# Optimization experiments

Hardware: AMD Instinct MI355X
Metric: run time of the kernel (lower is better)

## Reference

```python
import jax, jax.numpy as jnp
import numpy as np

BATCH = 256
SEQ_LEN = 512
INPUT_DIM = 1
NUM_HIDDEN = 2048
NUM_CLASSES = 10


def _xavier(key, shape):
    fan_out, fan_in = shape
    limit = np.sqrt(6.0 / (fan_in + fan_out)).astype(np.float32)
    return jax.random.uniform(key, shape, jnp.float32, -limit, limit)


def setup_inputs() -> dict:
    key = jax.random.key(0)
    kx, k1, k2, k3 = jax.random.split(key, 4)
    x = jax.random.normal(kx, (BATCH, SEQ_LEN), jnp.float32)
    wph = _xavier(k1, (NUM_CLASSES, NUM_HIDDEN))
    whh = _xavier(k2, (NUM_HIDDEN, NUM_HIDDEN))
    whx = _xavier(k3, (NUM_HIDDEN, INPUT_DIM))
    bh = jnp.zeros((NUM_HIDDEN,), jnp.float32)
    bp = jnp.zeros((NUM_CLASSES,), jnp.float32)
    return {"x": x, "whx": whx, "whh": whh, "bh": bh, "wph": wph, "bp": bp}


def reference(x, whx, whh, bh, wph, bp):
    # x: [B, T] of scalar inputs (input_dim == 1)
    B = x.shape[0]
    H = whh.shape[0]
    whx_vec = whx[:, 0]  # [H]

    def step(h, xt):
        # xt: [B];  xt[:, None] @ whx.T  ==  outer(xt, whx_vec)
        h_new = jnp.tanh(xt[:, None] * whx_vec[None, :] + h @ whh.T + bh)
        return h_new, None

    h0 = jnp.zeros((B, H), x.dtype)
    h_last, _ = jax.lax.scan(step, h0, x.T)  # scan over time: [T, B]
    p = h_last @ wph.T + bp  # [B, num_classes]
    return p
```

## Files before the change

kernel.cpp:

```cpp
#include <hip/hip_runtime.h>

#define SEQL   512
#define HID    2048
#define NCLS   10

typedef _Float16 f16x8 __attribute__((ext_vector_type(8)));
typedef float    f32x4 __attribute__((ext_vector_type(4)));
typedef unsigned uintx4 __attribute__((ext_vector_type(4)));

__device__ __forceinline__ float fast_tanh(float v) {
    float e = __expf(2.0f * v);
    return 1.0f - 2.0f / (e + 1.0f);
}

__global__ void pack_w_kernel(const float* __restrict__ w, _Float16* __restrict__ o) {
    const int fid = blockIdx.x * 256 + threadIdx.x;
    int col, k0;
    if (fid < 262144) {
        const int m = fid >> 13, s5 = fid & 8191;
        const int tile = s5 >> 12, kst = (s5 >> 6) & 63, ln = s5 & 63;
        col = m * 64 + tile * 16 + (ln & 15);
        k0  = kst * 32 + (ln >> 4) * 8;
    } else {
        const int q = fid - 262144;
        const int m = q >> 13, r = q & 8191;
        const int j = r >> 10, f = (r >> 6) & 15, ln = r & 63;
        col = m * 64 + 32 + (j & 1) * 16 + (ln & 15);
        k0  = ((j >> 1) * 16 + f) * 32 + (ln >> 4) * 8;
    }
    const float* src = w + (size_t)col * HID + k0;
    f16x8 v;
    #pragma unroll
    for (int i = 0; i < 8; ++i) v[i] = (_Float16)src[i];
    *(f16x8*)(o + (size_t)fid * 8) = v;
}

__global__ void __launch_bounds__(512, 2)
rnn_main(const float* __restrict__ x, const float* __restrict__ whx,
         const _Float16* __restrict__ Wp, const float* __restrict__ bh,
         const float* __restrict__ wph, const float* __restrict__ bp,
         _Float16* __restrict__ h0, _Float16* __restrict__ h1,
         unsigned* __restrict__ ctr, float* __restrict__ out)
{
    __shared__ uint4 ldsW[8192];
    __shared__ f32x4 ldsR[16 * 64];

    const int tid = threadIdx.x;

    int xcc;
    asm volatile("s_getreg_b32 %0, hwreg(HW_REG_XCC_ID)" : "=s"(xcc));
    const int g = xcc & 7;
    unsigned* alloc   = ctr + g * 64;
    unsigned* flgbase = ctr + 512 + g * 1024;
    if (tid == 0) {
        unsigned s = __hip_atomic_fetch_add(alloc, 1u, __ATOMIC_RELAXED, __HIP_MEMORY_SCOPE_WORKGROUP);
        ((unsigned*)ldsR)[0] = s;
    }
    __syncthreads();
    const int m = (int)((unsigned*)ldsR)[0];
    unsigned* myflg = flgbase + m * 32;
    const int rowbase = g * 32;
    const int colbase = m * 64;

    const int lane = tid & 63;
    const int j    = tid >> 6;
    const int cbb  = j & 1;
    const int kq   = j >> 1;

    const uint4* P4 = (const uint4*)Wp;

    for (int s5 = tid; s5 < 8192; s5 += 512)
        ldsW[s5] = P4[m * 8192 + s5];

    for (int i = tid; i < 32 * 64; i += 512) {
        const int r = i >> 6, c = i & 63;
        const int b = rowbase + r, jj = colbase + c;
        h0[(size_t)b * HID + jj] = (_Float16)fast_tanh(x[(size_t)b * SEQL] * whx[jj] + bh[jj]);
    }

    const uint4* R4 = P4 + 262144 + m * 8192 + j * 1024 + lane;
    f16x8 bR[16];
    #pragma unroll
    for (int f = 0; f < 16; ++f) bR[f] = *(const f16x8*)&R4[f * 64];

    const int ecls = (j >> 1) & 1, ewm = j >> 2;
    const int ecol = colbase + ecls * 32 + cbb * 16 + (lane & 15);
    const float wxc = whx[ecol], bbc = bh[ecol];
    const int erow = rowbase + ewm * 16 + (lane >> 4) * 4;
    const int rdbase = ecls * 8 + cbb * 4;

    const size_t aoff = (size_t)(rowbase + (lane & 15)) * HID + (lane >> 4) * 8 + kq * 16 * 32;
    const uint4* bl = &ldsW[cbb * 4096 + kq * 16 * 64 + lane];
    const unsigned* pollp = flgbase + (lane & 31) * 32;

    __syncthreads();
    if (tid == 0)
        __hip_atomic_fetch_add(myflg, 1u, __ATOMIC_RELAXED, __HIP_MEMORY_SCOPE_WORKGROUP);

    for (int t = 1; t < SEQL; ++t) {
        const _Float16* hs = (t & 1) ? h0 : h1;
        _Float16*       hd = (t & 1) ? h1 : h0;
        const _Float16* ap  = hs + aoff;
        const _Float16* ap1 = ap + 16 * HID;

        #pragma unroll
        for (int f = 0; f < 16; ++f) asm volatile("" : "+v"(bR[f]));

        float xv[4];
        #pragma unroll
        for (int r = 0; r < 4; ++r)
            xv[r] = x[(size_t)(erow + r) * SEQL + t];

        {
            unsigned v;
            do {
                v = __hip_atomic_load(pollp, __ATOMIC_RELAXED, __HIP_MEMORY_SCOPE_AGENT);
            } while (!__all((int)(v >= (unsigned)t)));
        }
        asm volatile("buffer_inv sc0" ::: "memory");

        uintx4 av0[16], av1[16];
        #pragma unroll
        for (int f = 0; f < 16; ++f) {
            asm volatile("global_load_dwordx4 %0, %1, off"
                         : "=v"(av0[f]) : "v"(ap + f * 32));
            asm volatile("global_load_dwordx4 %0, %1, off"
                         : "=v"(av1[f]) : "v"(ap1 + f * 32));
        }
        asm volatile("s_waitcnt vmcnt(0)" ::: "memory");
        __builtin_amdgcn_sched_barrier(0);

        f32x4 aL0 = {0.f,0.f,0.f,0.f}, aL1 = aL0, aR0 = aL0, aR1 = aL0;

        #pragma unroll
        for (int f = 0; f < 16; ++f) {
            const f16x8 a0 = __builtin_bit_cast(f16x8, av0[f]);
            const f16x8 a1 = __builtin_bit_cast(f16x8, av1[f]);
            const f16x8 bLf = *(const f16x8*)&bl[f * 64];
            aL0 = __builtin_amdgcn_mfma_f32_16x16x32_f16(a0, bLf,   aL0, 0, 0, 0);
            aL1 = __builtin_amdgcn_mfma_f32_16x16x32_f16(a1, bLf,   aL1, 0, 0, 0);
            aR0 = __builtin_amdgcn_mfma_f32_16x16x32_f16(a0, bR[f], aR0, 0, 0, 0);
            aR1 = __builtin_amdgcn_mfma_f32_16x16x32_f16(a1, bR[f], aR1, 0, 0, 0);
        }

        ldsR[(cbb * 4 + kq) * 64 + lane]       = aL0;
        ldsR[(8 + cbb * 4 + kq) * 64 + lane]   = aR0;
        __syncthreads();
        if (j < 4) {
            const f32x4 s = ldsR[(rdbase + 0) * 64 + lane] + ldsR[(rdbase + 1) * 64 + lane]
                          + ldsR[(rdbase + 2) * 64 + lane] + ldsR[(rdbase + 3) * 64 + lane];
            #pragma unroll
            for (int r = 0; r < 4; ++r) {
                const int br = erow + r;
                hd[(size_t)br * HID + ecol] =
                    (_Float16)fast_tanh(s[r] + xv[r] * wxc + bbc);
            }
        }
        __syncthreads();
        ldsR[(cbb * 4 + kq) * 64 + lane]       = aL1;
        ldsR[(8 + cbb * 4 + kq) * 64 + lane]   = aR1;
        __syncthreads();
        if (j >= 4) {
            const f32x4 s = ldsR[(rdbase + 0) * 64 + lane] + ldsR[(rdbase + 1) * 64 + lane]
                          + ldsR[(rdbase + 2) * 64 + lane] + ldsR[(rdbase + 3) * 64 + lane];
            #pragma unroll
            for (int r = 0; r < 4; ++r) {
                const int br = erow + r;
                hd[(size_t)br * HID + ecol] =
                    (_Float16)fast_tanh(s[r] + xv[r] * wxc + bbc);
            }
        }

        __syncthreads();
        if (tid == 0)
            __hip_atomic_fetch_add(myflg, 1u, __ATOMIC_RELAXED, __HIP_MEMORY_SCOPE_WORKGROUP);
    }

    {
        unsigned v;
        do {
            v = __hip_atomic_load(pollp, __ATOMIC_RELAXED, __HIP_MEMORY_SCOPE_AGENT);
        } while (!__all((int)(v >= (unsigned)SEQL)));
    }
    asm volatile("buffer_inv sc0" ::: "memory");

    const int brow = rowbase + m;
    const _Float16* hp = h1 + (size_t)brow * HID + lane * 32;
    for (int c = j; c < NCLS; c += 8) {
        const float* wp = wph + (size_t)c * HID + lane * 32;
        float psum = 0.f;
        #pragma unroll
        for (int i = 0; i < 32; ++i) psum += (float)hp[i] * wp[i];
        #pragma unroll
        for (int off = 32; off >= 1; off >>= 1) psum += __shfl_xor(psum, off, 64);
        if (lane == 0) out[brow * NCLS + c] = psum + bp[c];
    }
}

extern "C" void kernel_launch(void* const* d_in, const int* in_sizes, int n_in,
                              void* d_out, int out_size, void* d_ws, size_t ws_size,
                              hipStream_t stream) {
    const float* x   = (const float*)d_in[0];
    const float* whx = (const float*)d_in[1];
    const float* whh = (const float*)d_in[2];
    const float* bh  = (const float*)d_in[3];
    const float* wph = (const float*)d_in[4];
    const float* bp  = (const float*)d_in[5];
    float* out = (float*)d_out;

    char* ws = (char*)d_ws;
    _Float16* Wp  = (_Float16*)ws;
    _Float16* h0  = (_Float16*)(ws + (size_t)(8u << 20));
    _Float16* h1  = (_Float16*)(ws + (size_t)(9u << 20));
    unsigned* ctr = (unsigned*)(ws + (size_t)(10u << 20));

    hipMemsetAsync(ctr, 0, (512 + 8 * 1024) * sizeof(unsigned), stream);
    pack_w_kernel<<<dim3(2048), dim3(256), 0, stream>>>(whh, Wp);

    void* args[] = { (void*)&x, (void*)&whx, (void*)&Wp, (void*)&bh, (void*)&wph,
                     (void*)&bp, (void*)&h0, (void*)&h1, (void*)&ctr, (void*)&out };
    hipLaunchCooperativeKernel((const void*)rnn_main, dim3(256), dim3(512),
                               args, 0, stream);
}
```

Baseline: 4.764 ms.

## Split each timestep into two row-halves with separate flags to pipeline sync

New measurement: 4.380 ms (median of 2 runs). -8.1%, faster.

```diff
diff --git a/kernel.cpp b/kernel.cpp
--- a/kernel.cpp
+++ b/kernel.cpp
@@ -6,7 +6,6 @@
 
 typedef _Float16 f16x8 __attribute__((ext_vector_type(8)));
 typedef float    f32x4 __attribute__((ext_vector_type(4)));
-typedef unsigned uintx4 __attribute__((ext_vector_type(4)));
 
 __device__ __forceinline__ float fast_tanh(float v) {
     float e = __expf(2.0f * v);
@@ -44,21 +43,22 @@
 {
     __shared__ uint4 ldsW[8192];
     __shared__ f32x4 ldsR[16 * 64];
+    __shared__ unsigned s_mslot;
 
     const int tid = threadIdx.x;
 
     int xcc;
     asm volatile("s_getreg_b32 %0, hwreg(HW_REG_XCC_ID)" : "=s"(xcc));
     const int g = xcc & 7;
-    unsigned* alloc   = ctr + g * 64;
-    unsigned* flgbase = ctr + 512 + g * 1024;
-    if (tid == 0) {
-        unsigned s = __hip_atomic_fetch_add(alloc, 1u, __ATOMIC_RELAXED, __HIP_MEMORY_SCOPE_WORKGROUP);
-        ((unsigned*)ldsR)[0] = s;
-    }
+    unsigned* alloc = ctr + g * 64;
+    unsigned* flgA  = ctr + 512 + g * 1024;
+    unsigned* flgB  = ctr + 512 + 8192 + g * 1024;
+    if (tid == 0)
+        s_mslot = __hip_atomic_fetch_add(alloc, 1u, __ATOMIC_RELAXED, __HIP_MEMORY_SCOPE_WORKGROUP);
     __syncthreads();
-    const int m = (int)((unsigned*)ldsR)[0];
-    unsigned* myflg = flgbase + m * 32;
+    const int m = (int)s_mslot;
+    unsigned* myflgA = flgA + m * 32;
+    unsigned* myflgB = flgB + m * 32;
     const int rowbase = g * 32;
     const int colbase = m * 64;
 
@@ -83,104 +83,135 @@
     #pragma unroll
     for (int f = 0; f < 16; ++f) bR[f] = *(const f16x8*)&R4[f * 64];
 
-    const int ecls = (j >> 1) & 1, ewm = j >> 2;
-    const int ecol = colbase + ecls * 32 + cbb * 16 + (lane & 15);
+    const int tj   = (j < 4) ? j : j - 4;
+    const int ecls = tj >> 1, ecbb = tj & 1;
+    const int ecol = colbase + ecls * 32 + ecbb * 16 + (lane & 15);
     const float wxc = whx[ecol], bbc = bh[ecol];
-    const int erow = rowbase + ewm * 16 + (lane >> 4) * 4;
-    const int rdbase = ecls * 8 + cbb * 4;
-
-    const size_t aoff = (size_t)(rowbase + (lane & 15)) * HID + (lane >> 4) * 8 + kq * 16 * 32;
-    const uint4* bl = &ldsW[cbb * 4096 + kq * 16 * 64 + lane];
-    const unsigned* pollp = flgbase + (lane & 31) * 32;
+    const int eroff = (lane >> 4) * 4;
+    const int rdbase = tj * 4;
+
+    const size_t aoffA = (size_t)(rowbase + (lane & 15)) * HID + kq * 512 + (lane >> 4) * 8;
+    const size_t aoffB = aoffA + (size_t)16 * HID;
+    const uint4* bl = &ldsW[cbb * 4096 + kq * 1024 + lane];
+    const unsigned* pollA = flgA + (lane & 31) * 32;
+    const unsigned* pollB = flgB + (lane & 31) * 32;
 
     __syncthreads();
-    if (tid == 0)
-        __hip_atomic_fetch_add(myflg, 1u, __ATOMIC_RELAXED, __HIP_MEMORY_SCOPE_WORKGROUP);
+    if (tid == 0) {
+        __hip_atomic_fetch_add(myflgA, 4u, __ATOMIC_RELAXED, __HIP_MEMORY_SCOPE_WORKGROUP);
+        __hip_atomic_fetch_add(myflgB, 4u, __ATOMIC_RELAXED, __HIP_MEMORY_SCOPE_WORKGROUP);
+    }
 
     for (int t = 1; t < SEQL; ++t) {
         const _Float16* hs = (t & 1) ? h0 : h1;
         _Float16*       hd = (t & 1) ? h1 : h0;
-        const _Float16* ap  = hs + aoff;
-        const _Float16* ap1 = ap + 16 * HID;
+        const unsigned tgt = 4u * (unsigned)t;
 
         #pragma unroll
         for (int f = 0; f < 16; ++f) asm volatile("" : "+v"(bR[f]));
 
-        float xv[4];
-        #pragma unroll
-        for (int r = 0; r < 4; ++r)
-            xv[r] = x[(size_t)(erow + r) * SEQL + t];
-
         {
+            float xv[4];
+            if (j < 4) {
+                #pragma unroll
+                for (int r = 0; r < 4; ++r)
+                    xv[r] = x[(size_t)(rowbase + eroff + r) * SEQL + t];
+            }
             unsigned v;
             do {
-                v = __hip_atomic_load(pollp, __ATOMIC_RELAXED, __HIP_MEMORY_SCOPE_AGENT);
-            } while (!__all((int)(v >= (unsigned)t)));
+                v = __hip_atomic_load(pollA, __ATOMIC_RELAXED, __HIP_MEMORY_SCOPE_AGENT);
+            } while (!__all((int)(v >= tgt)));
+            asm volatile("buffer_inv sc0" ::: "memory");
+
+            f16x8 av[16];
+            #pragma unroll
+            for (int f = 0; f < 16; ++f)
+                av[f] = *(const f16x8*)(hs + aoffA + f * 32);
+
+            f32x4 aL = {0.f,0.f,0.f,0.f}, aR = aL;
+            #pragma unroll
+            for (int f = 0; f < 16; ++f) {
+                const f16x8 bLf = *(const f16x8*)&bl[f * 64];
+                aL = __builtin_amdgcn_mfma_f32_16x16x32_f16(av[f], bLf,   aL, 0, 0, 0);
+                aR = __builtin_amdgcn_mfma_f32_16x16x32_f16(av[f], bR[f], aR, 0, 0, 0);
+            }
+
+            __syncthreads();
+            ldsR[(cbb * 4 + kq) * 64 + lane]       = aL;
+            ldsR[((2 + cbb) * 4 + kq) * 64 + lane] = aR;
+            __syncthreads();
+
+            if (j < 4) {
+                const f32x4 s = ldsR[(rdbase + 0) * 64 + lane] + ldsR[(rdbase + 1) * 64 + lane]
+                              + ldsR[(rdbase + 2) * 64 + lane] + ldsR[(rdbase + 3) * 64 + lane];
+                #pragma unroll
+                for (int r = 0; r < 4; ++r) {
+                    const int br = rowbase + eroff + r;
+                    hd[(size_t)br * HID + ecol] =
+                        (_Float16)fast_tanh(s[r] + xv[r] * wxc + bbc);
+                }
+                asm volatile("s_waitcnt vmcnt(0)" ::: "memory");
+                if (lane == 0)
+                    __hip_atomic_fetch_add(myflgA, 1u, __ATOMIC_RELAXED, __HIP_MEMORY_SCOPE_WORKGROUP);
+            }
         }
-        asm volatile("buffer_inv sc0" ::: "memory");
-
-        uintx4 av0[16], av1[16];
-        #pragma unroll
-        for (int f = 0; f < 16; ++f) {
-            asm volatile("global_load_dwordx4 %0, %1, off"
-                         : "=v"(av0[f]) : "v"(ap + f * 32));
-            asm volatile("global_load_dwordx4 %0, %1, off"
-                         : "=v"(av1[f]) : "v"(ap1 + f * 32));
+
+        {
+            float xv[4];
+            if (j >= 4) {
+                #pragma unroll
+                for (int r = 0; r < 4; ++r)
+                    xv[r] = x[(size_t)(rowbase + 16 + eroff + r) * SEQL + t];
+            }
+            unsigned v;
+            do {
+                v = __hip_atomic_load(pollB, __ATOMIC_RELAXED, __HIP_MEMORY_SCOPE_AGENT);
+            } while (!__all((int)(v >= tgt)));
+            asm volatile("buffer_inv sc0" ::: "memory");
+
+            f16x8 av[16];
+            #pragma unroll
+            for (int f = 0; f < 16; ++f)
+                av[f] = *(const f16x8*)(hs + aoffB + f * 32);
+
+            f32x4 aL = {0.f,0.f,0.f,0.f}, aR = aL;
+            #pragma unroll
+            for (int f = 0; f < 16; ++f) {
+                const f16x8 bLf = *(const f16x8*)&bl[f * 64];
+                aL = __builtin_amdgcn_mfma_f32_16x16x32_f16(av[f], bLf,   aL, 0, 0, 0);
+                aR = __builtin_amdgcn_mfma_f32_16x16x32_f16(av[f], bR[f], aR, 0, 0, 0);
+            }
+
+            __syncthreads();
+            ldsR[(cbb * 4 + kq) * 64 + lane]       = aL;
+            ldsR[((2 + cbb) * 4 + kq) * 64 + lane] = aR;
+            __syncthreads();
+
+            if (j >= 4) {
+                const f32x4 s = ldsR[(rdbase + 0) * 64 + lane] + ldsR[(rdbase + 1) * 64 + lane]
+                              + ldsR[(rdbase + 2) * 64 + lane] + ldsR[(rdbase + 3) * 64 + lane];
+                #pragma unroll
+                for (int r = 0; r < 4; ++r) {
+                    const int br = rowbase + 16 + eroff + r;
+                    hd[(size_t)br * HID + ecol] =
+                        (_Float16)fast_tanh(s[r] + xv[r] * wxc + bbc);
+                }
+                asm volatile("s_waitcnt vmcnt(0)" ::: "memory");
+                if (lane == 0)
+                    __hip_atomic_fetch_add(myflgB, 1u, __ATOMIC_RELAXED, __HIP_MEMORY_SCOPE_WORKGROUP);
+            }
         }
-        asm volatile("s_waitcnt vmcnt(0)" ::: "memory");
-        __builtin_amdgcn_sched_barrier(0);
-
-        f32x4 aL0 = {0.f,0.f,0.f,0.f}, aL1 = aL0, aR0 = aL0, aR1 = aL0;
-
-        #pragma unroll
-        for (int f = 0; f < 16; ++f) {
-            const f16x8 a0 = __builtin_bit_cast(f16x8, av0[f]);
-            const f16x8 a1 = __builtin_bit_cast(f16x8, av1[f]);
-            const f16x8 bLf = *(const f16x8*)&bl[f * 64];
-            aL0 = __builtin_amdgcn_mfma_f32_16x16x32_f16(a0, bLf,   aL0, 0, 0, 0);
-            aL1 = __builtin_amdgcn_mfma_f32_16x16x32_f16(a1, bLf,   aL1, 0, 0, 0);
-            aR0 = __builtin_amdgcn_mfma_f32_16x16x32_f16(a0, bR[f], aR0, 0, 0, 0);
-            aR1 = __builtin_amdgcn_mfma_f32_16x16x32_f16(a1, bR[f], aR1, 0, 0, 0);
-        }
-
-        ldsR[(cbb * 4 + kq) * 64 + lane]       = aL0;
-        ldsR[(8 + cbb * 4 + kq) * 64 + lane]   = aR0;
-        __syncthreads();
-        if (j < 4) {
-            const f32x4 s = ldsR[(rdbase + 0) * 64 + lane] + ldsR[(rdbase + 1) * 64 + lane]
-                          + ldsR[(rdbase + 2) * 64 + lane] + ldsR[(rdbase + 3) * 64 + lane];
-            #pragma unroll
-            for (int r = 0; r < 4; ++r) {
-                const int br = erow + r;
-                hd[(size_t)br * HID + ecol] =
-                    (_Float16)fast_tanh(s[r] + xv[r] * wxc + bbc);
-            }
-        }
-        __syncthreads();
-        ldsR[(cbb * 4 + kq) * 64 + lane]       = aL1;
-        ldsR[(8 + cbb * 4 + kq) * 64 + lane]   = aR1;
-        __syncthreads();
-        if (j >= 4) {
-            const f32x4 s = ldsR[(rdbase + 0) * 64 + lane] + ldsR[(rdbase + 1) * 64 + lane]
-                          + ldsR[(rdbase + 2) * 64 + lane] + ldsR[(rdbase + 3) * 64 + lane];
-            #pragma unroll
-            for (int r = 0; r < 4; ++r) {
-                const int br = erow + r;
-                hd[(size_t)br * HID + ecol] =
-                    (_Float16)fast_tanh(s[r] + xv[r] * wxc + bbc);
-            }
-        }
-
-        __syncthreads();
-        if (tid == 0)
-            __hip_atomic_fetch_add(myflg, 1u, __ATOMIC_RELAXED, __HIP_MEMORY_SCOPE_WORKGROUP);
     }
 
     {
+        const unsigned tgt = 4u * (unsigned)SEQL;
         unsigned v;
         do {
-            v = __hip_atomic_load(pollp, __ATOMIC_RELAXED, __HIP_MEMORY_SCOPE_AGENT);
-        } while (!__all((int)(v >= (unsigned)SEQL)));
+            v = __hip_atomic_load(pollA, __ATOMIC_RELAXED, __HIP_MEMORY_SCOPE_AGENT);
+        } while (!__all((int)(v >= tgt)));
+        do {
+            v = __hip_atomic_load(pollB, __ATOMIC_RELAXED, __HIP_MEMORY_SCOPE_AGENT);
+        } while (!__all((int)(v >= tgt)));
     }
     asm volatile("buffer_inv sc0" ::: "memory");
 
@@ -214,7 +245,7 @@
     _Float16* h1  = (_Float16*)(ws + (size_t)(9u << 20));
     unsigned* ctr = (unsigned*)(ws + (size_t)(10u << 20));
 
-    hipMemsetAsync(ctr, 0, (512 + 8 * 1024) * sizeof(unsigned), stream);
+    hipMemsetAsync(ctr, 0, (512 + 2 * 8 * 1024) * sizeof(unsigned), stream);
     pack_w_kernel<<<dim3(2048), dim3(256), 0, stream>>>(whh, Wp);
 
     void* args[] = { (void*)&x, (void*)&whx, (void*)&Wp, (void*)&bh, (void*)&wph,
```
